# Performance work log

Hardware: AMD Instinct MI355X
Metric: run time of the kernel (lower is better)

The kernel has to match this reference:

```python
import jax, jax.numpy as jnp
import numpy as np

N = 500000      # nodes
F_IN = 10       # node_features
HID = 32        # DCRNN hidden
OUT = 2         # out_features
E = 8000000     # edges (unused in math since K=1, kept for interface fidelity)


def setup_inputs() -> dict:
    key = jax.random.key(0)
    ks = jax.random.split(key, 12)
    d_in = F_IN + HID  # 42: DConv input is cat([X, H])
    s = 0.1
    return {
        "x": jax.random.normal(ks[0], (N, F_IN), dtype=jnp.float32),
        "edge_index": jax.random.randint(ks[1], (2, E), 0, N, dtype=jnp.int64),
        "edge_weight": jax.random.uniform(ks[2], (E,), dtype=jnp.float32),
        "h": jax.random.normal(ks[3], (N, HID), dtype=jnp.float32),
        # DConv weights: torch shape (2, K=1, in, out); K dim squeezed -> (2, in, out)
        "W_z": jax.random.normal(ks[4], (2, d_in, HID), dtype=jnp.float32) * s,
        "b_z": jnp.zeros((HID,), dtype=jnp.float32),
        "W_r": jax.random.normal(ks[5], (2, d_in, HID), dtype=jnp.float32) * s,
        "b_r": jnp.zeros((HID,), dtype=jnp.float32),
        "W_h": jax.random.normal(ks[6], (2, d_in, HID), dtype=jnp.float32) * s,
        "b_h": jnp.zeros((HID,), dtype=jnp.float32),
        "W_lin": jax.random.normal(ks[7], (OUT, HID), dtype=jnp.float32) * s,
        "b_lin": jnp.zeros((OUT,), dtype=jnp.float32),
    }


def _dconv_k1(xh, W, b):
    # K=1 DConv: out/in diffusion weights collapse to a single dense transform
    return xh @ (W[0] + W[1]) + b


def reference(x, edge_index, edge_weight, h, W_z, b_z, W_r, b_r, W_h, b_h, W_lin, b_lin):
    # DCRNN GRU step (edge_index/edge_weight unused because K=1)
    xh = jnp.concatenate([x, h], axis=1)                  # [N, F_IN+HID]
    z = jax.nn.sigmoid(_dconv_k1(xh, W_z, b_z))           # update gate
    r = jax.nn.sigmoid(_dconv_k1(xh, W_r, b_r))           # reset gate
    xrh = jnp.concatenate([x, r * h], axis=1)
    h_tilde = jnp.tanh(_dconv_k1(xrh, W_h, b_h))
    h_new = z * h + (1.0 - z) * h_tilde                   # [N, HID]
    out = jnp.maximum(h_new, 0.0) @ W_lin.T + b_lin       # ReLU + Linear head, [N, OUT]
    return (out, h_new)
```

## Files before the change

### kernel.cpp

```cpp
#include <hip/hip_runtime.h>
#include <stdint.h>

static constexpr int N_NODES = 500000;
static constexpr int STR     = 56;

typedef __attribute__((ext_vector_type(8))) short short8;
typedef __attribute__((ext_vector_type(4))) float f32x4;


__device__ __forceinline__ float bfdec(uint32_t b){
  union{uint32_t u; float f;} c; c.u = b << 16; return c.f;
}
__device__ __forceinline__ float bf_lo(uint32_t u){ union{uint32_t u; float f;} c; c.u = u << 16; return c.f; }
__device__ __forceinline__ float bf_hi(uint32_t u){ union{uint32_t u; float f;} c; c.u = u & 0xffff0000u; return c.f; }
__device__ __forceinline__ uint32_t bfrne(float f){
  union{float f; uint32_t u;} c; c.f = f;
  return (c.u + 0x7fffu + ((c.u >> 16) & 1u)) >> 16;
}
__device__ __forceinline__ uint32_t pack2(float a, float b){
  return bfrne(a) | (bfrne(b) << 16);
}
__device__ __forceinline__ float sigmoid_fast(float x){
  float e = __expf(-x);
  return __builtin_amdgcn_rcpf(1.0f + e);
}
__device__ __forceinline__ float tanh_fast(float x){
  float e = __expf(2.0f * x);
  return 1.0f - 2.0f * __builtin_amdgcn_rcpf(e + 1.0f);
}

__device__ bool detect_f32_words(const uint32_t* w, int K){
  float m = 0.0f;
  for (int i = 0; i < K; i++) m = fmaxf(m, fabsf(bfdec(w[i] & 0xffffu)));
  return !(m < 1e6f);
}
__device__ __forceinline__ float wload(const void* p, int idx, bool f32w){
  if (f32w) return ((const float*)p)[idx];
  return bfdec(((const uint16_t*)p)[idx]);
}

__global__ void prep_kernel(const void* __restrict__ Wz,
                            const void* __restrict__ bz,
                            const void* __restrict__ Wr,
                            const void* __restrict__ br,
                            const void* __restrict__ Wh,
                            const void* __restrict__ bh,
                            const void* __restrict__ Wl,
                            const void* __restrict__ bl,
                            const uint32_t* __restrict__ xg,
                            const uint32_t* __restrict__ hg,
                            float* __restrict__ ws)
{
  const bool f32w = detect_f32_words((const uint32_t*)Wz, 64);
  uint16_t* wsh = (uint16_t*)ws;
  float*    wsf = ws;
  int i = blockIdx.x * 256 + threadIdx.x;
  if (i < 5376) {
    float v = 0.0f;
    if (i < 3584) {
      int col = i / STR, k = i - col * STR;
      if (k < 42) {
        const void* Wp = (col < 32) ? Wz : Wr;
        int j = (col < 32) ? col : col - 32;
        int src = k * 32 + j;
        v = wload(Wp, src, f32w) + wload(Wp, 1344 + src, f32w);
      }
    } else {
      int t2 = i - 3584;
      int col = t2 / STR, k = t2 - col * STR;
      if (k < 42) {
        int src = k * 32 + col;
        v = wload(Wh, src, f32w) + wload(Wh, 1344 + src, f32w);
      }
    }
    wsh[i] = (uint16_t)bfrne(v);
  } else if (i < 5538) {
    int r = i - 5376;
    if      (r < 32)  wsf[2688 + r]       = wload(bz, r,     f32w);
    else if (r < 64)  wsf[2720 + (r-32)]  = wload(br, r-32,  f32w);
    else if (r < 96)  wsf[2752 + (r-64)]  = wload(bh, r-64,  f32w);
    else if (r < 160) wsf[2784 + (r-96)]  = wload(Wl, r-96,  f32w);
    else              wsf[2848 + (r-160)] = wload(bl, r-160, f32w);
  } else if (i == 5568) {
    wsf[2850] = detect_f32_words(xg, 256) ? 1.0f : 0.0f;
  } else if (i == 5569) {
    wsf[2851] = detect_f32_words(hg, 256) ? 1.0f : 0.0f;
  }
}

__global__ __launch_bounds__(128, 4) void dcrnn_kernel(
    const uint32_t* __restrict__ xg,
    const uint32_t* __restrict__ hg,
    const float*    __restrict__ ws,
    float* __restrict__ out0,
    float* __restrict__ outh)
{
  __shared__ __align__(16) uint16_t xh_u16[128 * STR];

  const int t  = threadIdx.x;
  const int nd = blockIdx.x * 128 + t;
  const bool valid = nd < N_NODES;
  const float* wsf = ws;
  const uint16_t* wsh = (const uint16_t*)ws;
  const bool x_f32 = wsf[2850] != 0.0f;
  const bool h_f32 = wsf[2851] != 0.0f;

  uint32_t rw[24];
  #pragma unroll
  for (int i = 0; i < 24; i++) rw[i] = 0u;
  if (valid) {
    if (x_f32) {
      const float2* xr = (const float2*)((const float*)xg + (size_t)nd * 10);
      #pragma unroll
      for (int i = 0; i < 5; i++){ float2 v = xr[i]; rw[i] = pack2(v.x, v.y); }
    } else {
      const uint32_t* xr = xg + (size_t)nd * 5;
      #pragma unroll
      for (int i = 0; i < 5; i++) rw[i] = xr[i];
    }
    if (h_f32) {
      const float4* hr = (const float4*)((const float*)hg + (size_t)nd * 32);
      #pragma unroll
      for (int i = 0; i < 8; i++){
        float4 v = hr[i];
        rw[5 + 2*i]     = pack2(v.x, v.y);
        rw[5 + 2*i + 1] = pack2(v.z, v.w);
      }
    } else {
      const uint4* hr = (const uint4*)(hg + (size_t)nd * 16);
      #pragma unroll
      for (int i = 0; i < 4; i++){
        uint4 v = hr[i];
        rw[5 + 4*i]     = v.x; rw[5 + 4*i + 1] = v.y;
        rw[5 + 4*i + 2] = v.z; rw[5 + 4*i + 3] = v.w;
      }
    }
  }
  {
    uint4* dst = (uint4*)(xh_u16 + t * STR);
    #pragma unroll
    for (int c = 0; c < 6; c++)
      dst[c] = make_uint4(rw[4*c], rw[4*c+1], rw[4*c+2], rw[4*c+3]);
  }

  const int l = t & 63, w = t >> 6;
  const int lo16 = l & 15, g = l >> 4;
  const short8 zero8 = {0,0,0,0,0,0,0,0};

  short8 bzr_lo[4], bzr_hi[4];
  #pragma unroll
  for (int nt = 0; nt < 4; nt++){
    const uint16_t* brow = wsh + (nt*16 + lo16) * STR;
    bzr_lo[nt] = *(const short8*)(brow + g*8);
    bzr_hi[nt] = zero8;
    if (g < 2) bzr_hi[nt] = *(const short8*)(brow + 32 + g*8);
  }
  short8 bhf_lo[2], bhf_hi[2];
  #pragma unroll
  for (int nt = 0; nt < 2; nt++){
    const uint16_t* brow = wsh + 3584 + (nt*16 + lo16) * STR;
    bhf_lo[nt] = *(const short8*)(brow + g*8);
    bhf_hi[nt] = zero8;
    if (g < 2) bhf_hi[nt] = *(const short8*)(brow + 32 + g*8);
  }

  const float bzc0 = wsf[2688 + lo16], bzc1 = wsf[2704 + lo16];
  const float brc0 = wsf[2720 + lo16], brc1 = wsf[2736 + lo16];
  const float bhc0 = wsf[2752 + lo16], bhc1 = wsf[2768 + lo16];

  __syncthreads();

  uint16_t* xwm = xh_u16 + (w * 64) * STR;

  #pragma unroll
  for (int mt = 0; mt < 4; mt++){
    const uint16_t* arow = xwm + (mt*16 + lo16) * STR;
    short8 a0 = *(const short8*)(arow + g*8);
    short8 a1 = zero8;
    if (g < 2) a1 = *(const short8*)(arow + 32 + g*8);

    f32x4 accZ0 = {bzc0,bzc0,bzc0,bzc0};
    f32x4 accZ1 = {bzc1,bzc1,bzc1,bzc1};
    f32x4 accR0 = {brc0,brc0,brc0,brc0};
    f32x4 accR1 = {brc1,brc1,brc1,brc1};
    accZ0 = __builtin_amdgcn_mfma_f32_16x16x32_bf16(a0, bzr_lo[0], accZ0, 0,0,0);
    accZ0 = __builtin_amdgcn_mfma_f32_16x16x32_bf16(a1, bzr_hi[0], accZ0, 0,0,0);
    accZ1 = __builtin_amdgcn_mfma_f32_16x16x32_bf16(a0, bzr_lo[1], accZ1, 0,0,0);
    accZ1 = __builtin_amdgcn_mfma_f32_16x16x32_bf16(a1, bzr_hi[1], accZ1, 0,0,0);
    accR0 = __builtin_amdgcn_mfma_f32_16x16x32_bf16(a0, bzr_lo[2], accR0, 0,0,0);
    accR0 = __builtin_amdgcn_mfma_f32_16x16x32_bf16(a1, bzr_hi[2], accR0, 0,0,0);
    accR1 = __builtin_amdgcn_mfma_f32_16x16x32_bf16(a0, bzr_lo[3], accR1, 0,0,0);
    accR1 = __builtin_amdgcn_mfma_f32_16x16x32_bf16(a1, bzr_hi[3], accR1, 0,0,0);

    f32x4 hs0, hs1;
    #pragma unroll
    for (int q = 0; q < 4; q++){
      int row = mt*16 + g*4 + q;
      uint16_t* p0 = xwm + row*STR + 10 + lo16;
      uint16_t* p1 = xwm + row*STR + 26 + lo16;
      float h0 = bfdec(*p0), h1 = bfdec(*p1);
      float r0 = sigmoid_fast(accR0[q]);
      float r1 = sigmoid_fast(accR1[q]);
      *p0 = (uint16_t)bfrne(r0 * h0);
      *p1 = (uint16_t)bfrne(r1 * h1);
      hs0[q] = h0; hs1[q] = h1;
    }
    asm volatile("s_waitcnt lgkmcnt(0)" ::: "memory");

    f32x4 accH0 = {bhc0,bhc0,bhc0,bhc0};
    f32x4 accH1 = {bhc1,bhc1,bhc1,bhc1};
    short8 c0 = *(const short8*)(arow + g*8);
    short8 c1 = zero8;
    if (g < 2) c1 = *(const short8*)(arow + 32 + g*8);
    accH0 = __builtin_amdgcn_mfma_f32_16x16x32_bf16(c0, bhf_lo[0], accH0, 0,0,0);
    accH0 = __builtin_amdgcn_mfma_f32_16x16x32_bf16(c1, bhf_hi[0], accH0, 0,0,0);
    accH1 = __builtin_amdgcn_mfma_f32_16x16x32_bf16(c0, bhf_lo[1], accH1, 0,0,0);
    accH1 = __builtin_amdgcn_mfma_f32_16x16x32_bf16(c1, bhf_hi[1], accH1, 0,0,0);

    #pragma unroll
    for (int q = 0; q < 4; q++){
      int row  = mt*16 + g*4 + q;
      int node = blockIdx.x*128 + w*64 + row;
      float z0 = sigmoid_fast(accZ0[q]);
      float z1 = sigmoid_fast(accZ1[q]);
      float t0 = tanh_fast(accH0[q]);
      float t1 = tanh_fast(accH1[q]);
      float hn0 = fmaf(z0, hs0[q] - t0, t0);
      float hn1 = fmaf(z1, hs1[q] - t1, t1);
      if (node < N_NODES){
        outh[(size_t)node*32 + lo16]      = hn0;
        outh[(size_t)node*32 + 16 + lo16] = hn1;
      }
      *(xwm + row*STR + lo16)      = (uint16_t)bfrne(fmaxf(hn0, 0.0f));
      *(xwm + row*STR + 16 + lo16) = (uint16_t)bfrne(fmaxf(hn1, 0.0f));
    }
  }

  asm volatile("s_waitcnt lgkmcnt(0)" ::: "memory");
  if (valid){
    float o0 = wsf[2848], o1 = wsf[2849];
    const uint4* hq = (const uint4*)(xh_u16 + t * STR);
    #pragma unroll
    for (int i = 0; i < 4; i++){
      uint4 v = hq[i];
      uint32_t wv[4] = {v.x, v.y, v.z, v.w};
      #pragma unroll
      for (int j = 0; j < 4; j++){
        int c = i*8 + j*2;
        float v0 = bf_lo(wv[j]);
        float v1 = bf_hi(wv[j]);
        o0 = fmaf(v0, wsf[2784 + c],     o0);
        o1 = fmaf(v0, wsf[2816 + c],     o1);
        o0 = fmaf(v1, wsf[2784 + c + 1], o0);
        o1 = fmaf(v1, wsf[2816 + c + 1], o1);
      }
    }
    ((float2*)out0)[nd] = make_float2(o0, o1);
  }
}

extern "C" void kernel_launch(void* const* d_in, const int* in_sizes, int n_in,
                              void* d_out, int out_size, void* d_ws, size_t ws_size,
                              hipStream_t stream) {
  const uint32_t* x = (const uint32_t*)d_in[0];
  const uint32_t* h = (const uint32_t*)d_in[3];

  float* ws = (float*)d_ws;

  prep_kernel<<<22, 256, 0, stream>>>(d_in[4], d_in[5], d_in[6], d_in[7],
                                      d_in[8], d_in[9], d_in[10], d_in[11],
                                      x, h, ws);

  float* outf = (float*)d_out;
  float* out0 = outf;
  float* outh = outf + (size_t)2 * N_NODES;
  dcrnn_kernel<<<(N_NODES + 127) / 128, 128, 0, stream>>>(
      x, h, ws, out0, outh);
}
```

Before: 243.5 us.

## Split candidate GEMM into x/rh parts, interleave hidden columns, coalesce loads

Reorders weight columns so each lane owns an adjacent pair of hidden units, which allows packed 32-bit LDS accesses and float2 global stores via v_cvt_pk_bf16. The candidate-state GEMM is split into an x part, issued together with the z/r MFMAs, and an r*h part with K=32, which removes the serialised second pass over the 42-wide input. When inputs are bf16, a block-cooperative coalesced load path is added for x and h. Launch bounds occupancy drops from 4 to 2. Weight fragments are pinned in registers, and a redundant duplicate a0/a1 load appears in the loop.

```diff
diff --git a/kernel.cpp b/kernel.cpp
--- a/kernel.cpp
+++ b/kernel.cpp
@@ -19,6 +19,11 @@
 }
 __device__ __forceinline__ uint32_t pack2(float a, float b){
   return bfrne(a) | (bfrne(b) << 16);
+}
+__device__ __forceinline__ uint32_t cvtpk_bf16(float lo, float hi){
+  uint32_t r;
+  asm("v_cvt_pk_bf16_f32 %0, %1, %2" : "=v"(r) : "v"(lo), "v"(hi));
+  return r;
 }
 __device__ __forceinline__ float sigmoid_fast(float x){
   float e = __expf(-x);
@@ -56,39 +61,42 @@
   float*    wsf = ws;
   int i = blockIdx.x * 256 + threadIdx.x;
   if (i < 5376) {
+    int cc = i / STR, k = i - cc * STR;
+    int blk = cc >> 5, within = cc & 31;
+    int j = 2 * (within & 15) + (within >> 4);
     float v = 0.0f;
-    if (i < 3584) {
-      int col = i / STR, k = i - col * STR;
-      if (k < 42) {
-        const void* Wp = (col < 32) ? Wz : Wr;
-        int j = (col < 32) ? col : col - 32;
-        int src = k * 32 + j;
-        v = wload(Wp, src, f32w) + wload(Wp, 1344 + src, f32w);
-      }
+    if (blk == 0) {
+      if (k < 42) { int s = k*32 + j; v = wload(Wz, s, f32w) + wload(Wz, 1344 + s, f32w); }
+    } else if (blk == 1) {
+      if (k < 42) { int s = k*32 + j; v = wload(Wr, s, f32w) + wload(Wr, 1344 + s, f32w); }
     } else {
-      int t2 = i - 3584;
-      int col = t2 / STR, k = t2 - col * STR;
-      if (k < 42) {
-        int src = k * 32 + col;
-        v = wload(Wh, src, f32w) + wload(Wh, 1344 + src, f32w);
-      }
+      if (k < 10) { int s = k*32 + j; v = wload(Wh, s, f32w) + wload(Wh, 1344 + s, f32w); }
     }
     wsh[i] = (uint16_t)bfrne(v);
-  } else if (i < 5538) {
-    int r = i - 5376;
-    if      (r < 32)  wsf[2688 + r]       = wload(bz, r,     f32w);
-    else if (r < 64)  wsf[2720 + (r-32)]  = wload(br, r-32,  f32w);
-    else if (r < 96)  wsf[2752 + (r-64)]  = wload(bh, r-64,  f32w);
-    else if (r < 160) wsf[2784 + (r-96)]  = wload(Wl, r-96,  f32w);
-    else              wsf[2848 + (r-160)] = wload(bl, r-160, f32w);
-  } else if (i == 5568) {
-    wsf[2850] = detect_f32_words(xg, 256) ? 1.0f : 0.0f;
-  } else if (i == 5569) {
-    wsf[2851] = detect_f32_words(hg, 256) ? 1.0f : 0.0f;
-  }
-}
-
-__global__ __launch_bounds__(128, 4) void dcrnn_kernel(
+  } else if (i < 6400) {
+    int t2 = i - 5376;
+    int cc = t2 >> 5, k = t2 & 31;
+    int j = 2 * (cc & 15) + (cc >> 4);
+    int s = (10 + k)*32 + j;
+    wsh[i] = (uint16_t)bfrne(wload(Wh, s, f32w) + wload(Wh, 1344 + s, f32w));
+  } else if (i < 6496) {
+    int r = i - 6400;
+    int blk = r >> 5, within = r & 31;
+    int j = 2 * (within & 15) + (within >> 4);
+    const void* bp = (blk == 0) ? bz : (blk == 1) ? br : bh;
+    wsf[3200 + r] = wload(bp, j, f32w);
+  } else if (i < 6562) {
+    int r = i - 6496;
+    if (r < 64) wsf[3296 + r] = wload(Wl, r, f32w);
+    else        wsf[3360 + (r-64)] = wload(bl, r-64, f32w);
+  } else if (i == 6592) {
+    wsf[3362] = detect_f32_words(xg, 256) ? 1.0f : 0.0f;
+  } else if (i == 6593) {
+    wsf[3363] = detect_f32_words(hg, 256) ? 1.0f : 0.0f;
+  }
+}
+
+__global__ __launch_bounds__(128, 2) void dcrnn_kernel(
     const uint32_t* __restrict__ xg,
     const uint32_t* __restrict__ hg,
     const float*    __restrict__ ws,
@@ -102,71 +110,100 @@
   const bool valid = nd < N_NODES;
   const float* wsf = ws;
   const uint16_t* wsh = (const uint16_t*)ws;
-  const bool x_f32 = wsf[2850] != 0.0f;
-  const bool h_f32 = wsf[2851] != 0.0f;
-
-  uint32_t rw[24];
-  #pragma unroll
-  for (int i = 0; i < 24; i++) rw[i] = 0u;
-  if (valid) {
-    if (x_f32) {
-      const float2* xr = (const float2*)((const float*)xg + (size_t)nd * 10);
-      #pragma unroll
-      for (int i = 0; i < 5; i++){ float2 v = xr[i]; rw[i] = pack2(v.x, v.y); }
-    } else {
-      const uint32_t* xr = xg + (size_t)nd * 5;
-      #pragma unroll
-      for (int i = 0; i < 5; i++) rw[i] = xr[i];
-    }
-    if (h_f32) {
-      const float4* hr = (const float4*)((const float*)hg + (size_t)nd * 32);
-      #pragma unroll
-      for (int i = 0; i < 8; i++){
-        float4 v = hr[i];
-        rw[5 + 2*i]     = pack2(v.x, v.y);
-        rw[5 + 2*i + 1] = pack2(v.z, v.w);
+  const bool x_f32 = wsf[3362] != 0.0f;
+  const bool h_f32 = wsf[3363] != 0.0f;
+
+  if (x_f32 || h_f32) {
+    uint32_t rw[24];
+    #pragma unroll
+    for (int i = 0; i < 24; i++) rw[i] = 0u;
+    if (valid) {
+      if (x_f32) {
+        const float2* xr = (const float2*)((const float*)xg + (size_t)nd * 10);
+        #pragma unroll
+        for (int i = 0; i < 5; i++){ float2 v = xr[i]; rw[i] = pack2(v.x, v.y); }
+      } else {
+        const uint32_t* xr = xg + (size_t)nd * 5;
+        #pragma unroll
+        for (int i = 0; i < 5; i++) rw[i] = xr[i];
       }
-    } else {
-      const uint4* hr = (const uint4*)(hg + (size_t)nd * 16);
-      #pragma unroll
-      for (int i = 0; i < 4; i++){
-        uint4 v = hr[i];
-        rw[5 + 4*i]     = v.x; rw[5 + 4*i + 1] = v.y;
-        rw[5 + 4*i + 2] = v.z; rw[5 + 4*i + 3] = v.w;
+      if (h_f32) {
+        const float4* hr = (const float4*)((const float*)hg + (size_t)nd * 32);
+        #pragma unroll
+        for (int i = 0; i < 8; i++){
+          float4 v = hr[i];
+          rw[5 + 2*i]     = pack2(v.x, v.y);
+          rw[5 + 2*i + 1] = pack2(v.z, v.w);
+        }
+      } else {
+        const uint4* hr = (const uint4*)(hg + (size_t)nd * 16);
+        #pragma unroll
+        for (int i = 0; i < 4; i++){
+          uint4 v = hr[i];
+          rw[5 + 4*i] = v.x; rw[5 + 4*i + 1] = v.y;
+          rw[5 + 4*i + 2] = v.z; rw[5 + 4*i + 3] = v.w;
+        }
       }
     }
-  }
-  {
     uint4* dst = (uint4*)(xh_u16 + t * STR);
     #pragma unroll
     for (int c = 0; c < 6; c++)
       dst[c] = make_uint4(rw[4*c], rw[4*c+1], rw[4*c+2], rw[4*c+3]);
+  } else {
+    const uint32_t* xbase = xg + (size_t)blockIdx.x * 640;
+    #pragma unroll
+    for (int i = 0; i < 5; i++){
+      int idx = i * 128 + t;
+      uint32_t v = 0u;
+      if ((size_t)blockIdx.x * 640 + idx < (size_t)N_NODES * 5) v = xbase[idx];
+      int node = (idx * 6554) >> 15;
+      int col  = idx - node * 5;
+      *(uint32_t*)(xh_u16 + node * STR + col * 2) = v;
+    }
+    const uint4* hbase = (const uint4*)(hg + (size_t)blockIdx.x * 2048);
+    #pragma unroll
+    for (int i = 0; i < 4; i++){
+      int idx = i * 128 + t;
+      uint4 v = make_uint4(0u,0u,0u,0u);
+      if ((size_t)blockIdx.x * 512 + idx < (size_t)N_NODES * 4) v = hbase[idx];
+      int node = idx >> 2, chunk = idx & 3;
+      *(uint4*)(xh_u16 + node * STR + 10 + chunk * 8) = v;
+    }
+    *(uint32_t*)(xh_u16 + t * STR + 42) = 0u;
+    *(uint32_t*)(xh_u16 + t * STR + 44) = 0u;
+    *(uint32_t*)(xh_u16 + t * STR + 46) = 0u;
   }
 
   const int l = t & 63, w = t >> 6;
   const int lo16 = l & 15, g = l >> 4;
   const short8 zero8 = {0,0,0,0,0,0,0,0};
 
-  short8 bzr_lo[4], bzr_hi[4];
+  short8 b_lo[6], b_hi[4];
+  #pragma unroll
+  for (int nt = 0; nt < 6; nt++){
+    const uint16_t* brow = wsh + (nt*16 + lo16) * STR;
+    b_lo[nt] = *(const short8*)(brow + g*8);
+  }
   #pragma unroll
   for (int nt = 0; nt < 4; nt++){
     const uint16_t* brow = wsh + (nt*16 + lo16) * STR;
-    bzr_lo[nt] = *(const short8*)(brow + g*8);
-    bzr_hi[nt] = zero8;
-    if (g < 2) bzr_hi[nt] = *(const short8*)(brow + 32 + g*8);
-  }
-  short8 bhf_lo[2], bhf_hi[2];
+    b_hi[nt] = (g < 2) ? *(const short8*)(brow + 32 + g*8) : zero8;
+  }
+  short8 bhh[2];
   #pragma unroll
   for (int nt = 0; nt < 2; nt++){
-    const uint16_t* brow = wsh + 3584 + (nt*16 + lo16) * STR;
-    bhf_lo[nt] = *(const short8*)(brow + g*8);
-    bhf_hi[nt] = zero8;
-    if (g < 2) bhf_hi[nt] = *(const short8*)(brow + 32 + g*8);
-  }
-
-  const float bzc0 = wsf[2688 + lo16], bzc1 = wsf[2704 + lo16];
-  const float brc0 = wsf[2720 + lo16], brc1 = wsf[2736 + lo16];
-  const float bhc0 = wsf[2752 + lo16], bhc1 = wsf[2768 + lo16];
+    const uint16_t* brow = wsh + 5376 + (nt*16 + lo16) * 32;
+    bhh[nt] = *(const short8*)(brow + g*8);
+  }
+  #pragma unroll
+  for (int nt = 0; nt < 6; nt++) asm("" : "+v"(b_lo[nt]));
+  #pragma unroll
+  for (int nt = 0; nt < 4; nt++) asm("" : "+v"(b_hi[nt]));
+  asm("" : "+v"(bhh[0]), "+v"(bhh[1]));
+
+  const float bzc0 = wsf[3200 + lo16], bzc1 = wsf[3216 + lo16];
+  const float brc0 = wsf[3232 + lo16], brc1 = wsf[3248 + lo16];
+  const float bhc0 = wsf[3264 + lo16], bhc1 = wsf[3280 + lo16];
 
   __syncthreads();
 
@@ -174,48 +211,46 @@
 
   #pragma unroll
   for (int mt = 0; mt < 4; mt++){
-    const uint16_t* arow = xwm + (mt*16 + lo16) * STR;
-    short8 a0 = *(const short8*)(arow + g*8);
+    uint16_t* arow = xwm + (mt*16 + lo16) * STR;
+    short8 a0 = *(const short8*)(arow);
     short8 a1 = zero8;
+    if (g < 2) a1 = *(const short8*)(arow + 32);
+    a0 = *(const short8*)(arow + g*8);
     if (g < 2) a1 = *(const short8*)(arow + 32 + g*8);
 
     f32x4 accZ0 = {bzc0,bzc0,bzc0,bzc0};
     f32x4 accZ1 = {bzc1,bzc1,bzc1,bzc1};
     f32x4 accR0 = {brc0,brc0,brc0,brc0};
     f32x4 accR1 = {brc1,brc1,brc1,brc1};
-    accZ0 = __builtin_amdgcn_mfma_f32_16x16x32_bf16(a0, bzr_lo[0], accZ0, 0,0,0);
-    accZ0 = __builtin_amdgcn_mfma_f32_16x16x32_bf16(a1, bzr_hi[0], accZ0, 0,0,0);
-    accZ1 = __builtin_amdgcn_mfma_f32_16x16x32_bf16(a0, bzr_lo[1], accZ1, 0,0,0);
-    accZ1 = __builtin_amdgcn_mfma_f32_16x16x32_bf16(a1, bzr_hi[1], accZ1, 0,0,0);
-    accR0 = __builtin_amdgcn_mfma_f32_16x16x32_bf16(a0, bzr_lo[2], accR0, 0,0,0);
-    accR0 = __builtin_amdgcn_mfma_f32_16x16x32_bf16(a1, bzr_hi[2], accR0, 0,0,0);
-    accR1 = __builtin_amdgcn_mfma_f32_16x16x32_bf16(a0, bzr_lo[3], accR1, 0,0,0);
-    accR1 = __builtin_amdgcn_mfma_f32_16x16x32_bf16(a1, bzr_hi[3], accR1, 0,0,0);
+    f32x4 accH0 = {bhc0,bhc0,bhc0,bhc0};
+    f32x4 accH1 = {bhc1,bhc1,bhc1,bhc1};
+    accZ0 = __builtin_amdgcn_mfma_f32_16x16x32_bf16(a0, b_lo[0], accZ0, 0,0,0);
+    accZ0 = __builtin_amdgcn_mfma_f32_16x16x32_bf16(a1, b_hi[0], accZ0, 0,0,0);
+    accZ1 = __builtin_amdgcn_mfma_f32_16x16x32_bf16(a0, b_lo[1], accZ1, 0,0,0);
+    accZ1 = __builtin_amdgcn_mfma_f32_16x16x32_bf16(a1, b_hi[1], accZ1, 0,0,0);
+    accR0 = __builtin_amdgcn_mfma_f32_16x16x32_bf16(a0, b_lo[2], accR0, 0,0,0);
+    accR0 = __builtin_amdgcn_mfma_f32_16x16x32_bf16(a1, b_hi[2], accR0, 0,0,0);
+    accR1 = __builtin_amdgcn_mfma_f32_16x16x32_bf16(a0, b_lo[3], accR1, 0,0,0);
+    accR1 = __builtin_amdgcn_mfma_f32_16x16x32_bf16(a1, b_hi[3], accR1, 0,0,0);
+    accH0 = __builtin_amdgcn_mfma_f32_16x16x32_bf16(a0, b_lo[4], accH0, 0,0,0);
+    accH1 = __builtin_amdgcn_mfma_f32_16x16x32_bf16(a0, b_lo[5], accH1, 0,0,0);
 
     f32x4 hs0, hs1;
     #pragma unroll
     for (int q = 0; q < 4; q++){
       int row = mt*16 + g*4 + q;
-      uint16_t* p0 = xwm + row*STR + 10 + lo16;
-      uint16_t* p1 = xwm + row*STR + 26 + lo16;
-      float h0 = bfdec(*p0), h1 = bfdec(*p1);
+      uint32_t hp = *(const uint32_t*)(xwm + row*STR + 10 + 2*lo16);
+      float h0 = bf_lo(hp), h1 = bf_hi(hp);
       float r0 = sigmoid_fast(accR0[q]);
       float r1 = sigmoid_fast(accR1[q]);
-      *p0 = (uint16_t)bfrne(r0 * h0);
-      *p1 = (uint16_t)bfrne(r1 * h1);
+      *(uint32_t*)(xwm + row*STR + 2*lo16) = cvtpk_bf16(r0*h0, r1*h1);
       hs0[q] = h0; hs1[q] = h1;
     }
     asm volatile("s_waitcnt lgkmcnt(0)" ::: "memory");
 
-    f32x4 accH0 = {bhc0,bhc0,bhc0,bhc0};
-    f32x4 accH1 = {bhc1,bhc1,bhc1,bhc1};
-    short8 c0 = *(const short8*)(arow + g*8);
-    short8 c1 = zero8;
-    if (g < 2) c1 = *(const short8*)(arow + 32 + g*8);
-    accH0 = __builtin_amdgcn_mfma_f32_16x16x32_bf16(c0, bhf_lo[0], accH0, 0,0,0);
-    accH0 = __builtin_amdgcn_mfma_f32_16x16x32_bf16(c1, bhf_hi[0], accH0, 0,0,0);
-    accH1 = __builtin_amdgcn_mfma_f32_16x16x32_bf16(c0, bhf_lo[1], accH1, 0,0,0);
-    accH1 = __builtin_amdgcn_mfma_f32_16x16x32_bf16(c1, bhf_hi[1], accH1, 0,0,0);
+    short8 aR = *(const short8*)(arow + g*8);
+    accH0 = __builtin_amdgcn_mfma_f32_16x16x32_bf16(aR, bhh[0], accH0, 0,0,0);
+    accH1 = __builtin_amdgcn_mfma_f32_16x16x32_bf16(aR, bhh[1], accH1, 0,0,0);
 
     #pragma unroll
     for (int q = 0; q < 4; q++){
@@ -227,32 +262,30 @@
       float t1 = tanh_fast(accH1[q]);
       float hn0 = fmaf(z0, hs0[q] - t0, t0);
       float hn1 = fmaf(z1, hs1[q] - t1, t1);
-      if (node < N_NODES){
-        outh[(size_t)node*32 + lo16]      = hn0;
-        outh[(size_t)node*32 + 16 + lo16] = hn1;
-      }
-      *(xwm + row*STR + lo16)      = (uint16_t)bfrne(fmaxf(hn0, 0.0f));
-      *(xwm + row*STR + 16 + lo16) = (uint16_t)bfrne(fmaxf(hn1, 0.0f));
+      if (node < N_NODES)
+        *(float2*)(outh + (size_t)node*32 + 2*lo16) = make_float2(hn0, hn1);
+      *(uint32_t*)(xwm + row*STR + 2*lo16) =
+          cvtpk_bf16(fmaxf(hn0, 0.0f), fmaxf(hn1, 0.0f));
     }
   }
 
   asm volatile("s_waitcnt lgkmcnt(0)" ::: "memory");
   if (valid){
-    float o0 = wsf[2848], o1 = wsf[2849];
+    float o0 = wsf[3360], o1 = wsf[3361];
     const uint4* hq = (const uint4*)(xh_u16 + t * STR);
     #pragma unroll
     for (int i = 0; i < 4; i++){
       uint4 v = hq[i];
       uint32_t wv[4] = {v.x, v.y, v.z, v.w};
       #pragma unroll
-      for (int j = 0; j < 4; j++){
-        int c = i*8 + j*2;
-        float v0 = bf_lo(wv[j]);
-        float v1 = bf_hi(wv[j]);
-        o0 = fmaf(v0, wsf[2784 + c],     o0);
-        o1 = fmaf(v0, wsf[2816 + c],     o1);
-        o0 = fmaf(v1, wsf[2784 + c + 1], o0);
-        o1 = fmaf(v1, wsf[2816 + c + 1], o1);
+      for (int p = 0; p < 4; p++){
+        int j = i*8 + p*2;
+        float v0 = bf_lo(wv[p]);
+        float v1 = bf_hi(wv[p]);
+        o0 = fmaf(v0, wsf[3296 + j],     o0);
+        o1 = fmaf(v0, wsf[3328 + j],     o1);
+        o0 = fmaf(v1, wsf[3296 + j + 1], o0);
+        o1 = fmaf(v1, wsf[3328 + j + 1], o1);
       }
     }
     ((float2*)out0)[nd] = make_float2(o0, o1);
@@ -267,7 +300,7 @@
 
   float* ws = (float*)d_ws;
 
-  prep_kernel<<<22, 256, 0, stream>>>(d_in[4], d_in[5], d_in[6], d_in[7],
+  prep_kernel<<<26, 256, 0, stream>>>(d_in[4], d_in[5], d_in[6], d_in[7],
                                       d_in[8], d_in[9], d_in[10], d_in[11],
                                       x, h, ws);
 
```

Measured after the change: 242.7 us. Within noise of the previous version (-0.3%).
